# Optimization experiments

Measured on AMD Instinct MI355X. Metric: run time of the kernel, lower is better.

Reference implementation:

```python
import jax, jax.numpy as jnp
import numpy as np

B, LA, LB = 16, 2048, 2048
DA, DB, DH = 768, 512, 512
EPS = 1e-5


def _layer_norm(x, g, b):
    mu = jnp.mean(x, axis=-1, keepdims=True)
    var = jnp.var(x, axis=-1, keepdims=True)
    return (x - mu) * jax.lax.rsqrt(var + EPS) * g + b


def setup_inputs() -> dict:
    key = jax.random.key(0)
    ks = jax.random.split(key, 12)
    s = lambda d: 1.0 / np.sqrt(d)
    return {
        "z_a": jax.random.normal(ks[0], (B, LA, DA), jnp.float32),
        "z_b": jax.random.normal(ks[1], (B, LB, DB), jnp.float32),
        "Wa": jax.random.uniform(ks[2], (DA, DH), jnp.float32, -s(DA), s(DA)),
        "ba": jnp.zeros((DH,), jnp.float32),
        "Wb": jax.random.uniform(ks[3], (DB, DH), jnp.float32, -s(DB), s(DB)),
        "bb": jnp.zeros((DH,), jnp.float32),
        "W_co": jax.random.normal(ks[4], (DH, DH), jnp.float32),
        "Woa": jax.random.uniform(ks[5], (DH, DA), jnp.float32, -s(DH), s(DH)),
        "boa": jnp.zeros((DA,), jnp.float32),
        "Wob": jax.random.uniform(ks[6], (DH, DB), jnp.float32, -s(DH), s(DH)),
        "bob": jnp.zeros((DB,), jnp.float32),
        "ga": jnp.ones((DA,), jnp.float32),
        "beta_a": jnp.zeros((DA,), jnp.float32),
        "gb": jnp.ones((DB,), jnp.float32),
        "beta_b": jnp.zeros((DB,), jnp.float32),
    }


def reference(z_a, z_b, Wa, ba, Wb, bb, W_co, Woa, boa, Wob, bob, ga, beta_a, gb, beta_b):
    # projections to shared hidden space
    h_a = jnp.einsum('bld,dh->blh', z_a, Wa) + ba          # (B, LA, DH)
    h_b = jnp.einsum('bld,dh->blh', z_b, Wb) + bb          # (B, LB, DH)
    # bilinear tanh co-attention scores
    C = jnp.tanh(jnp.einsum('bih,hk,bjk->bij', h_a, W_co, h_b))  # (B, LA, LB)
    attn_a = jax.nn.softmax(C, axis=-1)                    # rows: over LB
    attn_b = jax.nn.softmax(C.transpose(0, 2, 1), axis=-1) # cols: over LA
    h_a_co = jnp.einsum('bij,bjh->bih', attn_a, h_b)       # (B, LA, DH)
    h_b_co = jnp.einsum('bji,bih->bjh', attn_b, h_a)       # (B, LB, DH)
    z_a_co = jnp.einsum('blh,hd->bld', h_a_co, Woa) + boa
    z_b_co = jnp.einsum('blh,hd->bld', h_b_co, Wob) + bob
    z_a_out = _layer_norm(z_a + z_a_co, ga, beta_a)
    z_b_out = _layer_norm(z_b + z_b_co, gb, beta_b)
    return (z_a_out, z_b_out)
```

## Files before the change

### kernel.cpp

```cpp
#include <hip/hip_runtime.h>
#include <stdint.h>

typedef short bf16x8 __attribute__((ext_vector_type(8)));
typedef float f32x16 __attribute__((ext_vector_type(16)));

#define BM 256
#define BN 256
#define BK 64
#define ABUF_U 16384
#define BUF_U  32768

#define AS1 __attribute__((address_space(1)))
#define AS3 __attribute__((address_space(3)))

__device__ __forceinline__ ushort f2bf(float x) {
    uint32_t u = __float_as_uint(x);
    u += 0x7FFFu + ((u >> 16) & 1u);
    return (ushort)(u >> 16);
}

__device__ __forceinline__ void gload16(const void* g, void* l) {
    __builtin_amdgcn_global_load_lds((const AS1 void*)g, (AS3 void*)l, 16, 0, 0);
}

#define ISSUE2(kt, buf, i0)                                                          \
    do {                                                                             \
        gload16(((i0) < 4 ? Ap : Bp) + goff[i0] + (kt), smem + (buf)*BUF_U + loff[i0]); \
        gload16((((i0)+1) < 4 ? Ap : Bp) + goff[(i0)+1] + (kt), smem + (buf)*BUF_U + loff[(i0)+1]); \
    } while (0)

template<int MODE, bool HAS_BIAS, bool WRITE_T>
__global__ __launch_bounds__(512, 2)
void gemm_bt(const ushort* __restrict__ Aptr_, const ushort* __restrict__ Bptr_,
             void* __restrict__ Cptr_, ushort* __restrict__ CTptr_,
             const float* __restrict__ bias, const float* __restrict__ resid_,
             float* __restrict__ rsum_, float* __restrict__ csum_,
             const float* __restrict__ scale_,
             int M, int N, int K, int lda, int ldb, int ldc,
             long sA, long sB, long sC, long sCT, long sSum,
             int ldct, int rbshift)
{
    extern __shared__ ushort smem[];

    const int gx = gridDim.x, gy = gridDim.y;
    const int nwg = gx * gy * (int)gridDim.z;
    int flat = ((int)blockIdx.z * gy + (int)blockIdx.y) * gx + (int)blockIdx.x;
    {
        const int q8 = nwg >> 3, r8 = nwg & 7;
        const int xcd = flat & 7, loc = flat >> 3;
        flat = (xcd < r8 ? xcd * (q8 + 1) : r8 * (q8 + 1) + (xcd - r8) * q8) + loc;
    }
    const int z   = flat / (gx * gy);
    const int rem = flat - z * (gx * gy);
    const int m0  = (rem % gx) * BM;
    const int n0  = (rem / gx) * BN;

    const int tid  = threadIdx.x;
    const int lane = tid & 63;
    const int wave = tid >> 6;
    const int wr   = wave >> 2;
    const int wcn  = wave & 3;
    const int lr   = lane & 31, lh = lane >> 5;

    const ushort* Ap = Aptr_ + z * sA;
    const ushort* Bp = Bptr_ + z * sB;

    long goff[8]; int loff[8];
    #pragma unroll
    for (int u = 0; u < 4; ++u) {
        const int li  = u * 512 + tid;
        const int row = li >> 3;
        const int gck = (li & 7) ^ (row & 7);
        goff[u]     = (long)(m0 + row) * lda + gck * 8;
        loff[u]     = li * 8;
        goff[u + 4] = (long)(n0 + row) * ldb + gck * 8;
        loff[u + 4] = ABUF_U + li * 8;
    }

    f32x16 acc[4][2] = {};

    const int nk = K / BK;
    ISSUE2(0, 0, 0); ISSUE2(0, 0, 2); ISSUE2(0, 0, 4); ISSUE2(0, 0, 6);

    for (int t = 0; t < nk; ++t) {
        const int cur = t & 1, nxt = cur ^ 1;
        const ushort* As = smem + cur * BUF_U;
        const ushort* Bs = As + ABUF_U;
        const bool pf = (t + 1 < nk);
        const int kt1 = (t + 1) * BK;

        if (pf) {
            ISSUE2(kt1, nxt, 0);
            asm volatile("s_waitcnt vmcnt(2)" ::: "memory");
        } else {
            asm volatile("s_waitcnt vmcnt(0)" ::: "memory");
        }
        __builtin_amdgcn_s_barrier();

        #pragma unroll
        for (int kk = 0; kk < 4; ++kk) {
            bf16x8 af[4], bfv[2];
            #pragma unroll
            for (int tm = 0; tm < 4; ++tm) {
                const int row = wr * 128 + tm * 32 + lr;
                const int ck  = (kk * 2 + lh) ^ (row & 7);
                af[tm] = *(const bf16x8*)&As[row * BK + ck * 8];
            }
            #pragma unroll
            for (int tn = 0; tn < 2; ++tn) {
                const int row = wcn * 64 + tn * 32 + lr;
                const int ck  = (kk * 2 + lh) ^ (row & 7);
                bfv[tn] = *(const bf16x8*)&Bs[row * BK + ck * 8];
            }
            if (pf) {
                if (kk == 0)      ISSUE2(kt1, nxt, 2);
                else if (kk == 1) ISSUE2(kt1, nxt, 4);
                else if (kk == 2) ISSUE2(kt1, nxt, 6);
            }
            #pragma unroll
            for (int tm = 0; tm < 4; ++tm)
                #pragma unroll
                for (int tn = 0; tn < 2; ++tn)
                    acc[tm][tn] = __builtin_amdgcn_mfma_f32_32x32x16_bf16(
                        af[tm], bfv[tn], acc[tm][tn], 0, 0, 0);
        }

        asm volatile("s_waitcnt lgkmcnt(0)" ::: "memory");
        __builtin_amdgcn_s_barrier();
    }

    const int colb0 = n0 + wcn * 64 + lr;
    const int rowbw = m0 + wr * 128 + 4 * lh;

    if constexpr (MODE == 3) {
        float* Co = (float*)Cptr_;
        #pragma unroll
        for (int tm = 0; tm < 4; ++tm)
            #pragma unroll
            for (int tn = 0; tn < 2; ++tn) {
                const int col = colb0 + tn * 32;
                const float bv = bias[col];
                #pragma unroll
                for (int q = 0; q < 4; ++q)
                    #pragma unroll
                    for (int s = 0; s < 4; ++s) {
                        const int row = rowbw + tm * 32 + q * 8 + s;
                        const long idx = (long)row * ldc + col;
                        Co[idx] = acc[tm][tn][q * 4 + s] + bv + resid_[idx];
                    }
            }
    } else if constexpr (MODE == 0) {
        ushort* Cp = (ushort*)Cptr_ + z * sC;
        #pragma unroll
        for (int tm = 0; tm < 4; ++tm)
            #pragma unroll
            for (int tn = 0; tn < 2; ++tn) {
                const int col = colb0 + tn * 32;
                const float bv = HAS_BIAS ? bias[col] : 0.f;
                ushort us[16];
                #pragma unroll
                for (int rr = 0; rr < 16; ++rr) us[rr] = f2bf(acc[tm][tn][rr] + bv);
                #pragma unroll
                for (int q = 0; q < 4; ++q)
                    #pragma unroll
                    for (int s = 0; s < 4; ++s)
                        Cp[(long)(rowbw + tm * 32 + q * 8 + s) * ldc + col] = us[q * 4 + s];
                if constexpr (WRITE_T) {
                    #pragma unroll
                    for (int q = 0; q < 4; ++q) {
                        const int gr = rowbw + tm * 32 + q * 8;
                        const int bb = gr >> rbshift;
                        const int ii = gr & ((1 << rbshift) - 1);
                        *(ushort4*)&CTptr_[(long)bb * sCT + (long)col * ldct + ii] =
                            make_ushort4(us[q * 4 + 0], us[q * 4 + 1], us[q * 4 + 2], us[q * 4 + 3]);
                    }
                }
            }
    } else if constexpr (MODE == 1) {
        ushort* Ep  = (ushort*)Cptr_ + z * sC;
        ushort* ETp = CTptr_ + z * sCT;
        float* rs = rsum_ + z * sSum;
        float* cs = csum_ + z * sSum;
        float colp[2] = {0.f, 0.f};
        #pragma unroll
        for (int tm = 0; tm < 4; ++tm) {
            float rowp[16];
            #pragma unroll
            for (int rr = 0; rr < 16; ++rr) rowp[rr] = 0.f;
            #pragma unroll
            for (int tn = 0; tn < 2; ++tn) {
                const int col = colb0 + tn * 32;
                ushort us[16];
                #pragma unroll
                for (int rr = 0; rr < 16; ++rr) {
                    const float x  = acc[tm][tn][rr];
                    const float th = 1.f - 2.f / (__expf(2.f * x) + 1.f);
                    const float e  = __expf(th);
                    rowp[rr] += e;
                    colp[tn] += e;
                    us[rr] = f2bf(e);
                }
                #pragma unroll
                for (int q = 0; q < 4; ++q) {
                    #pragma unroll
                    for (int s = 0; s < 4; ++s)
                        Ep[(long)(rowbw + tm * 32 + q * 8 + s) * ldc + col] = us[q * 4 + s];
                    const int gr = rowbw + tm * 32 + q * 8;
                    *(ushort4*)&ETp[(long)col * ldct + gr] =
                        make_ushort4(us[q * 4 + 0], us[q * 4 + 1], us[q * 4 + 2], us[q * 4 + 3]);
                }
            }
            #pragma unroll
            for (int rr = 0; rr < 16; ++rr) {
                float v = rowp[rr];
                v += __shfl_xor(v, 1);  v += __shfl_xor(v, 2);
                v += __shfl_xor(v, 4);  v += __shfl_xor(v, 8);
                v += __shfl_xor(v, 16);
                if (lr == 0)
                    atomicAdd(&rs[rowbw + tm * 32 + (rr & 3) + 8 * (rr >> 2)], v);
            }
        }
        #pragma unroll
        for (int tn = 0; tn < 2; ++tn) {
            float v = colp[tn];
            v += __shfl_xor(v, 32);
            if (lh == 0) atomicAdd(&cs[colb0 + tn * 32], v);
        }
    } else {
        const float* sc = scale_ + z * sSum;
        ushort* Cp = (ushort*)Cptr_ + z * sC;
        #pragma unroll
        for (int tm = 0; tm < 4; ++tm) {
            float rcp[16];
            #pragma unroll
            for (int rr = 0; rr < 16; ++rr)
                rcp[rr] = 1.f / sc[rowbw + tm * 32 + (rr & 3) + 8 * (rr >> 2)];
            #pragma unroll
            for (int tn = 0; tn < 2; ++tn) {
                const int col = colb0 + tn * 32;
                #pragma unroll
                for (int q = 0; q < 4; ++q)
                    #pragma unroll
                    for (int s = 0; s < 4; ++s)
                        Cp[(long)(rowbw + tm * 32 + q * 8 + s) * ldc + col] =
                            f2bf(acc[tm][tn][q * 4 + s] * rcp[q * 4 + s]);
            }
        }
    }
}

__global__ __launch_bounds__(256)
void cast32to16(const float* __restrict__ in, ushort* __restrict__ out, long n) {
    const long stride = (long)gridDim.x * 256 * 8;
    for (long i = ((long)blockIdx.x * 256 + threadIdx.x) * 8; i < n; i += stride) {
        const float4 f0 = *(const float4*)(in + i);
        const float4 f1 = *(const float4*)(in + i + 4);
        uint4 w;
        w.x = (uint)f2bf(f0.x) | ((uint)f2bf(f0.y) << 16);
        w.y = (uint)f2bf(f0.z) | ((uint)f2bf(f0.w) << 16);
        w.z = (uint)f2bf(f1.x) | ((uint)f2bf(f1.y) << 16);
        w.w = (uint)f2bf(f1.z) | ((uint)f2bf(f1.w) << 16);
        *(uint4*)(out + i) = w;
    }
}

__global__ __launch_bounds__(256)
void tcast(const float* __restrict__ in, ushort* __restrict__ out, int R, int C) {
    __shared__ float t[32][33];
    const int bx = blockIdx.x * 32, by = blockIdx.y * 32;
    const int tx = threadIdx.x, ty = threadIdx.y;
    for (int i = ty; i < 32; i += 8) {
        const int r = by + i, cc = bx + tx;
        if (r < R && cc < C) t[i][tx] = in[(long)r * C + cc];
    }
    __syncthreads();
    for (int i = ty; i < 32; i += 8) {
        const int cc = bx + i, r = by + tx;
        if (cc < C && r < R) out[(long)cc * R + r] = f2bf(t[tx][i]);
    }
}

template<int D>
__global__ __launch_bounds__(256)
void ln_rows(float* __restrict__ y, const float* __restrict__ gam, const float* __restrict__ bet) {
    constexpr int NV = D / 256;
    const long row = blockIdx.x;
    float* p = y + row * D;
    const int tid = threadIdx.x;
    float v[NV];
    float s = 0.f, s2 = 0.f;
    #pragma unroll
    for (int k = 0; k < NV; ++k) {
        v[k] = p[tid + k * 256];
        s += v[k]; s2 += v[k] * v[k];
    }
    #pragma unroll
    for (int off = 1; off < 64; off <<= 1) {
        s  += __shfl_xor(s, off);
        s2 += __shfl_xor(s2, off);
    }
    __shared__ float ws[4], ws2[4];
    const int wave = tid >> 6, lane = tid & 63;
    if (lane == 0) { ws[wave] = s; ws2[wave] = s2; }
    __syncthreads();
    s  = ws[0] + ws[1] + ws[2] + ws[3];
    s2 = ws2[0] + ws2[1] + ws2[2] + ws2[3];
    const float mu  = s / D;
    const float var = s2 / D - mu * mu;
    const float rstd = rsqrtf(var + 1e-5f);
    #pragma unroll
    for (int k = 0; k < NV; ++k) {
        const int i = tid + k * 256;
        p[i] = (v[k] - mu) * rstd * gam[i] + bet[i];
    }
}

extern "C" void kernel_launch(void* const* d_in, const int* in_sizes, int n_in,
                              void* d_out, int out_size, void* d_ws, size_t ws_size,
                              hipStream_t stream)
{
    (void)in_sizes; (void)n_in; (void)out_size; (void)ws_size;
    const float* z_a    = (const float*)d_in[0];
    const float* z_b    = (const float*)d_in[1];
    const float* Wa     = (const float*)d_in[2];
    const float* ba     = (const float*)d_in[3];
    const float* Wb     = (const float*)d_in[4];
    const float* bb     = (const float*)d_in[5];
    const float* Wco    = (const float*)d_in[6];
    const float* Woa    = (const float*)d_in[7];
    const float* boa    = (const float*)d_in[8];
    const float* Wob    = (const float*)d_in[9];
    const float* bob    = (const float*)d_in[10];
    const float* ga     = (const float*)d_in[11];
    const float* beta_a = (const float*)d_in[12];
    const float* gb     = (const float*)d_in[13];
    const float* beta_b = (const float*)d_in[14];

    const int Bn = 16, LA = 2048, LB = 2048, DA = 768, DB = 512, DH = 512;
    const long MA = (long)Bn * LA;
    const long MB = (long)Bn * LB;

    char* w = (char*)d_ws;
    size_t off = 0;
    auto alc = [&](size_t bytes) { void* p = w + off; off += (bytes + 255) & ~(size_t)255; return p; };

    ushort* WaT  = (ushort*)alc((size_t)DH * DA * 2);
    ushort* WbT  = (ushort*)alc((size_t)DH * DB * 2);
    ushort* WcoT = (ushort*)alc((size_t)DH * DH * 2);
    ushort* WoaT = (ushort*)alc((size_t)DA * DH * 2);
    ushort* WobT = (ushort*)alc((size_t)DB * DH * 2);
    ushort* h_a  = (ushort*)alc((size_t)MA * DH * 2);
    ushort* h_b  = (ushort*)alc((size_t)MB * DH * 2);
    ushort* h_aT = (ushort*)alc((size_t)Bn * DH * LA * 2);
    ushort* h_bT = (ushort*)alc((size_t)Bn * DH * LB * 2);
    ushort* Ma   = (ushort*)alc((size_t)MA * DH * 2);
    ushort* E    = (ushort*)alc((size_t)Bn * LA * LB * 2);
    ushort* ET   = (ushort*)alc((size_t)Bn * LB * LA * 2);
    ushort* Pa   = (ushort*)alc((size_t)MA * DH * 2);
    ushort* Pb   = (ushort*)alc((size_t)MB * DH * 2);
    float*  rsum = (float*)alc((size_t)Bn * LA * 4);
    float*  csum = (float*)alc((size_t)Bn * LB * 4);

    ushort* za16 = E;
    ushort* zb16 = E + (size_t)MA * DA;

    dim3 blk(512, 1, 1);
    dim3 blk256(256, 1, 1);
    dim3 tb(32, 8, 1);
    const int SHM = 2 * BUF_U * 2;

    tcast<<<dim3(DH / 32, DA / 32, 1), tb, 0, stream>>>(Wa,  WaT,  DA, DH);
    tcast<<<dim3(DH / 32, DB / 32, 1), tb, 0, stream>>>(Wb,  WbT,  DB, DH);
    tcast<<<dim3(DH / 32, DH / 32, 1), tb, 0, stream>>>(Wco, WcoT, DH, DH);
    tcast<<<dim3(DA / 32, DH / 32, 1), tb, 0, stream>>>(Woa, WoaT, DH, DA);
    tcast<<<dim3(DB / 32, DH / 32, 1), tb, 0, stream>>>(Wob, WobT, DH, DB);

    cast32to16<<<dim3(2048, 1, 1), blk256, 0, stream>>>(z_a, za16, MA * DA);
    cast32to16<<<dim3(2048, 1, 1), blk256, 0, stream>>>(z_b, zb16, MB * DB);

    hipMemsetAsync(rsum, 0, (size_t)Bn * (LA + LB) * sizeof(float), stream);

    gemm_bt<0, true, true><<<dim3(MA / BM, DH / BN, 1), blk, SHM, stream>>>(
        za16, WaT, h_a, h_aT, ba, nullptr, nullptr, nullptr, nullptr,
        (int)MA, DH, DA, DA, DA, DH, 0, 0, 0, (long)DH * LA, 0, LA, 11);

    gemm_bt<0, true, true><<<dim3(MB / BM, DH / BN, 1), blk, SHM, stream>>>(
        zb16, WbT, h_b, h_bT, bb, nullptr, nullptr, nullptr, nullptr,
        (int)MB, DH, DB, DB, DB, DH, 0, 0, 0, (long)DH * LB, 0, LB, 11);

    gemm_bt<0, false, false><<<dim3(MA / BM, DH / BN, 1), blk, SHM, stream>>>(
        h_a, WcoT, Ma, nullptr, nullptr, nullptr, nullptr, nullptr, nullptr,
        (int)MA, DH, DH, DH, DH, DH, 0, 0, 0, 0, 0, 0, 0);

    gemm_bt<1, false, false><<<dim3(LA / BM, LB / BN, Bn), blk, SHM, stream>>>(
        Ma, h_b, E, ET, nullptr, nullptr, rsum, csum, nullptr,
        LA, LB, DH, DH, DH, LB,
        (long)LA * DH, (long)LB * DH, (long)LA * LB, (long)LB * LA, LA, LA, 0);

    gemm_bt<2, false, false><<<dim3(LA / BM, DH / BN, Bn), blk, SHM, stream>>>(
        E, h_bT, Pa, nullptr, nullptr, nullptr, nullptr, nullptr, rsum,
        LA, DH, LB, LB, LB, DH,
        (long)LA * LB, (long)DH * LB, (long)LA * DH, 0, LA, 0, 0);

    gemm_bt<2, false, false><<<dim3(LB / BM, DH / BN, Bn), blk, SHM, stream>>>(
        ET, h_aT, Pb, nullptr, nullptr, nullptr, nullptr, nullptr, csum,
        LB, DH, LA, LA, LA, DH,
        (long)LB * LA, (long)DH * LA, (long)LB * DH, 0, LB, 0, 0);

    float* outA = (float*)d_out;
    float* outB = outA + MA * DA;

    gemm_bt<3, true, false><<<dim3(MA / BM, DA / BN, 1), blk, SHM, stream>>>(
        Pa, WoaT, outA, nullptr, boa, z_a, nullptr, nullptr, nullptr,
        (int)MA, DA, DH, DH, DH, DA, 0, 0, 0, 0, 0, 0, 0);

    gemm_bt<3, true, false><<<dim3(MB / BM, DB / BN, 1), blk, SHM, stream>>>(
        Pb, WobT, outB, nullptr, bob, z_b, nullptr, nullptr, nullptr,
        (int)MB, DB, DH, DH, DH, DB, 0, 0, 0, 0, 0, 0, 0);

    ln_rows<768><<<dim3((unsigned)MA, 1, 1), blk256, 0, stream>>>(outA, ga, beta_a);
    ln_rows<512><<<dim3((unsigned)MB, 1, 1), blk256, 0, stream>>>(outB, gb, beta_b);
}
```

Baseline: 704.6 us.

## Shrink GEMM tiles to 128x128 without prefetch and keep the residual path in bf16

The GEMM kernel drops from 256x256 tiles with 512 threads and a double-buffered async-LDS prefetch pipeline to 128x128 tiles with 256 threads, static single-buffered LDS, and plain syncthreads around each K step. The output projection now writes a bf16 pre-norm sum, using the bf16-cast input as the residual. A new vectorized layernorm kernel reads that bf16 buffer and writes the float result. These changes cut fp32 traffic in the epilogue and layernorm, but they give up load/compute overlap, raise the number of workgroups and redundant operand loads, and lower the accuracy of the residual and the pre-norm sum.

```diff
diff --git a/kernel.cpp b/kernel.cpp
--- a/kernel.cpp
+++ b/kernel.cpp
@@ -4,11 +4,9 @@
 typedef short bf16x8 __attribute__((ext_vector_type(8)));
 typedef float f32x16 __attribute__((ext_vector_type(16)));
 
-#define BM 256
-#define BN 256
+#define BM 128
+#define BN 128
 #define BK 64
-#define ABUF_U 16384
-#define BUF_U  32768
 
 #define AS1 __attribute__((address_space(1)))
 #define AS3 __attribute__((address_space(3)))
@@ -18,29 +16,27 @@
     u += 0x7FFFu + ((u >> 16) & 1u);
     return (ushort)(u >> 16);
 }
+__device__ __forceinline__ float bf2f(ushort u) {
+    return __uint_as_float((uint)u << 16);
+}
 
 __device__ __forceinline__ void gload16(const void* g, void* l) {
     __builtin_amdgcn_global_load_lds((const AS1 void*)g, (AS3 void*)l, 16, 0, 0);
 }
 
-#define ISSUE2(kt, buf, i0)                                                          \
-    do {                                                                             \
-        gload16(((i0) < 4 ? Ap : Bp) + goff[i0] + (kt), smem + (buf)*BUF_U + loff[i0]); \
-        gload16((((i0)+1) < 4 ? Ap : Bp) + goff[(i0)+1] + (kt), smem + (buf)*BUF_U + loff[(i0)+1]); \
-    } while (0)
-
 template<int MODE, bool HAS_BIAS, bool WRITE_T>
-__global__ __launch_bounds__(512, 2)
+__global__ __launch_bounds__(256)
 void gemm_bt(const ushort* __restrict__ Aptr_, const ushort* __restrict__ Bptr_,
              void* __restrict__ Cptr_, ushort* __restrict__ CTptr_,
-             const float* __restrict__ bias, const float* __restrict__ resid_,
+             const float* __restrict__ bias, const ushort* __restrict__ resid_,
              float* __restrict__ rsum_, float* __restrict__ csum_,
              const float* __restrict__ scale_,
              int M, int N, int K, int lda, int ldb, int ldc,
              long sA, long sB, long sC, long sCT, long sSum,
              int ldct, int rbshift)
 {
-    extern __shared__ ushort smem[];
+    __shared__ ushort Alds[BM * BK];
+    __shared__ ushort Blds[BN * BK];
 
     const int gx = gridDim.x, gy = gridDim.y;
     const int nwg = gx * gy * (int)gridDim.z;
@@ -58,84 +54,66 @@
     const int tid  = threadIdx.x;
     const int lane = tid & 63;
     const int wave = tid >> 6;
-    const int wr   = wave >> 2;
-    const int wcn  = wave & 3;
+    const int wr   = wave >> 1;
+    const int wcn  = wave & 1;
     const int lr   = lane & 31, lh = lane >> 5;
 
     const ushort* Ap = Aptr_ + z * sA;
     const ushort* Bp = Bptr_ + z * sB;
 
-    long goff[8]; int loff[8];
+    long aoff[4], boff[4]; int lofs[4];
     #pragma unroll
     for (int u = 0; u < 4; ++u) {
-        const int li  = u * 512 + tid;
+        const int li  = u * 256 + tid;
         const int row = li >> 3;
         const int gck = (li & 7) ^ (row & 7);
-        goff[u]     = (long)(m0 + row) * lda + gck * 8;
-        loff[u]     = li * 8;
-        goff[u + 4] = (long)(n0 + row) * ldb + gck * 8;
-        loff[u + 4] = ABUF_U + li * 8;
-    }
-
-    f32x16 acc[4][2] = {};
-
-    const int nk = K / BK;
-    ISSUE2(0, 0, 0); ISSUE2(0, 0, 2); ISSUE2(0, 0, 4); ISSUE2(0, 0, 6);
-
-    for (int t = 0; t < nk; ++t) {
-        const int cur = t & 1, nxt = cur ^ 1;
-        const ushort* As = smem + cur * BUF_U;
-        const ushort* Bs = As + ABUF_U;
-        const bool pf = (t + 1 < nk);
-        const int kt1 = (t + 1) * BK;
-
-        if (pf) {
-            ISSUE2(kt1, nxt, 0);
-            asm volatile("s_waitcnt vmcnt(2)" ::: "memory");
-        } else {
-            asm volatile("s_waitcnt vmcnt(0)" ::: "memory");
+        aoff[u] = (long)(m0 + row) * lda + gck * 8;
+        boff[u] = (long)(n0 + row) * ldb + gck * 8;
+        lofs[u] = li * 8;
+    }
+
+    f32x16 acc[2][2] = {};
+
+    for (int kt = 0; kt < K; kt += BK) {
+        #pragma unroll
+        for (int u = 0; u < 4; ++u) {
+            gload16(Ap + aoff[u] + kt, &Alds[lofs[u]]);
+            gload16(Bp + boff[u] + kt, &Blds[lofs[u]]);
         }
-        __builtin_amdgcn_s_barrier();
+        __syncthreads();
 
         #pragma unroll
         for (int kk = 0; kk < 4; ++kk) {
-            bf16x8 af[4], bfv[2];
-            #pragma unroll
-            for (int tm = 0; tm < 4; ++tm) {
-                const int row = wr * 128 + tm * 32 + lr;
+            bf16x8 af[2], bfv[2];
+            #pragma unroll
+            for (int tm = 0; tm < 2; ++tm) {
+                const int row = wr * 64 + tm * 32 + lr;
                 const int ck  = (kk * 2 + lh) ^ (row & 7);
-                af[tm] = *(const bf16x8*)&As[row * BK + ck * 8];
+                af[tm] = *(const bf16x8*)&Alds[row * BK + ck * 8];
             }
             #pragma unroll
             for (int tn = 0; tn < 2; ++tn) {
                 const int row = wcn * 64 + tn * 32 + lr;
                 const int ck  = (kk * 2 + lh) ^ (row & 7);
-                bfv[tn] = *(const bf16x8*)&Bs[row * BK + ck * 8];
-            }
-            if (pf) {
-                if (kk == 0)      ISSUE2(kt1, nxt, 2);
-                else if (kk == 1) ISSUE2(kt1, nxt, 4);
-                else if (kk == 2) ISSUE2(kt1, nxt, 6);
-            }
-            #pragma unroll
-            for (int tm = 0; tm < 4; ++tm)
+                bfv[tn] = *(const bf16x8*)&Blds[row * BK + ck * 8];
+            }
+            #pragma unroll
+            for (int tm = 0; tm < 2; ++tm)
                 #pragma unroll
                 for (int tn = 0; tn < 2; ++tn)
                     acc[tm][tn] = __builtin_amdgcn_mfma_f32_32x32x16_bf16(
                         af[tm], bfv[tn], acc[tm][tn], 0, 0, 0);
         }
-
-        asm volatile("s_waitcnt lgkmcnt(0)" ::: "memory");
-        __builtin_amdgcn_s_barrier();
+        __syncthreads();
     }
 
     const int colb0 = n0 + wcn * 64 + lr;
-    const int rowbw = m0 + wr * 128 + 4 * lh;
+    const int rowbw = m0 + wr * 64 + 4 * lh;
 
     if constexpr (MODE == 3) {
-        float* Co = (float*)Cptr_;
-        #pragma unroll
-        for (int tm = 0; tm < 4; ++tm)
+        ushort* Cp = (ushort*)Cptr_;
+        #pragma unroll
+        for (int tm = 0; tm < 2; ++tm)
             #pragma unroll
             for (int tn = 0; tn < 2; ++tn) {
                 const int col = colb0 + tn * 32;
@@ -146,13 +124,13 @@
                     for (int s = 0; s < 4; ++s) {
                         const int row = rowbw + tm * 32 + q * 8 + s;
                         const long idx = (long)row * ldc + col;
-                        Co[idx] = acc[tm][tn][q * 4 + s] + bv + resid_[idx];
+                        Cp[idx] = f2bf(acc[tm][tn][q * 4 + s] + bv + bf2f(resid_[idx]));
                     }
             }
     } else if constexpr (MODE == 0) {
         ushort* Cp = (ushort*)Cptr_ + z * sC;
         #pragma unroll
-        for (int tm = 0; tm < 4; ++tm)
+        for (int tm = 0; tm < 2; ++tm)
             #pragma unroll
             for (int tn = 0; tn < 2; ++tn) {
                 const int col = colb0 + tn * 32;
@@ -183,7 +161,7 @@
         float* cs = csum_ + z * sSum;
         float colp[2] = {0.f, 0.f};
         #pragma unroll
-        for (int tm = 0; tm < 4; ++tm) {
+        for (int tm = 0; tm < 2; ++tm) {
             float rowp[16];
             #pragma unroll
             for (int rr = 0; rr < 16; ++rr) rowp[rr] = 0.f;
@@ -230,7 +208,7 @@
         const float* sc = scale_ + z * sSum;
         ushort* Cp = (ushort*)Cptr_ + z * sC;
         #pragma unroll
-        for (int tm = 0; tm < 4; ++tm) {
+        for (int tm = 0; tm < 2; ++tm) {
             float rcp[16];
             #pragma unroll
             for (int rr = 0; rr < 16; ++rr)
@@ -281,19 +259,16 @@
 }
 
 template<int D>
-__global__ __launch_bounds__(256)
-void ln_rows(float* __restrict__ y, const float* __restrict__ gam, const float* __restrict__ bet) {
-    constexpr int NV = D / 256;
+__global__ __launch_bounds__(D / 4)
+void ln_bf(const ushort* __restrict__ y, float* __restrict__ out,
+           const float* __restrict__ gam, const float* __restrict__ bet) {
+    constexpr int NW = D / 256;
     const long row = blockIdx.x;
-    float* p = y + row * D;
     const int tid = threadIdx.x;
-    float v[NV];
-    float s = 0.f, s2 = 0.f;
-    #pragma unroll
-    for (int k = 0; k < NV; ++k) {
-        v[k] = p[tid + k * 256];
-        s += v[k]; s2 += v[k] * v[k];
-    }
+    const ushort4 v4 = *(const ushort4*)&y[row * D + tid * 4];
+    float v[4] = {bf2f(v4.x), bf2f(v4.y), bf2f(v4.z), bf2f(v4.w)};
+    float s = v[0] + v[1] + v[2] + v[3];
+    float s2 = v[0]*v[0] + v[1]*v[1] + v[2]*v[2] + v[3]*v[3];
     #pragma unroll
     for (int off = 1; off < 64; off <<= 1) {
         s  += __shfl_xor(s, off);
@@ -303,16 +278,20 @@
     const int wave = tid >> 6, lane = tid & 63;
     if (lane == 0) { ws[wave] = s; ws2[wave] = s2; }
     __syncthreads();
-    s  = ws[0] + ws[1] + ws[2] + ws[3];
-    s2 = ws2[0] + ws2[1] + ws2[2] + ws2[3];
-    const float mu  = s / D;
-    const float var = s2 / D - mu * mu;
+    s = 0.f; s2 = 0.f;
+    #pragma unroll
+    for (int w2 = 0; w2 < NW; ++w2) { s += ws[w2]; s2 += ws2[w2]; }
+    const float mu   = s / D;
+    const float var  = s2 / D - mu * mu;
     const float rstd = rsqrtf(var + 1e-5f);
-    #pragma unroll
-    for (int k = 0; k < NV; ++k) {
-        const int i = tid + k * 256;
-        p[i] = (v[k] - mu) * rstd * gam[i] + bet[i];
-    }
+    const float4 gv = *(const float4*)&gam[tid * 4];
+    const float4 bv = *(const float4*)&bet[tid * 4];
+    float4 o;
+    o.x = (v[0] - mu) * rstd * gv.x + bv.x;
+    o.y = (v[1] - mu) * rstd * gv.y + bv.y;
+    o.z = (v[2] - mu) * rstd * gv.z + bv.z;
+    o.w = (v[3] - mu) * rstd * gv.w + bv.w;
+    *(float4*)&out[row * D + tid * 4] = o;
 }
 
 extern "C" void kernel_launch(void* const* d_in, const int* in_sizes, int n_in,
@@ -361,13 +340,13 @@
     float*  rsum = (float*)alc((size_t)Bn * LA * 4);
     float*  csum = (float*)alc((size_t)Bn * LB * 4);
 
-    ushort* za16 = E;
-    ushort* zb16 = E + (size_t)MA * DA;
-
-    dim3 blk(512, 1, 1);
-    dim3 blk256(256, 1, 1);
+    ushort* za16 = (ushort*)d_out;
+    ushort* zb16 = za16 + (size_t)MA * DA;
+    ushort* yA = E;
+    ushort* yB = E + (size_t)MA * DA;
+
+    dim3 blk(256, 1, 1);
     dim3 tb(32, 8, 1);
-    const int SHM = 2 * BUF_U * 2;
 
     tcast<<<dim3(DH / 32, DA / 32, 1), tb, 0, stream>>>(Wa,  WaT,  DA, DH);
     tcast<<<dim3(DH / 32, DB / 32, 1), tb, 0, stream>>>(Wb,  WbT,  DB, DH);
@@ -375,49 +354,48 @@
     tcast<<<dim3(DA / 32, DH / 32, 1), tb, 0, stream>>>(Woa, WoaT, DH, DA);
     tcast<<<dim3(DB / 32, DH / 32, 1), tb, 0, stream>>>(Wob, WobT, DH, DB);
 
-    cast32to16<<<dim3(2048, 1, 1), blk256, 0, stream>>>(z_a, za16, MA * DA);
-    cast32to16<<<dim3(2048, 1, 1), blk256, 0, stream>>>(z_b, zb16, MB * DB);
+    cast32to16<<<dim3(2048, 1, 1), blk, 0, stream>>>(z_a, za16, MA * DA);
+    cast32to16<<<dim3(2048, 1, 1), blk, 0, stream>>>(z_b, zb16, MB * DB);
 
     hipMemsetAsync(rsum, 0, (size_t)Bn * (LA + LB) * sizeof(float), stream);
 
-    gemm_bt<0, true, true><<<dim3(MA / BM, DH / BN, 1), blk, SHM, stream>>>(
+    gemm_bt<0, true, true><<<dim3(MA / BM, DH / BN, 1), blk, 0, stream>>>(
         za16, WaT, h_a, h_aT, ba, nullptr, nullptr, nullptr, nullptr,
         (int)MA, DH, DA, DA, DA, DH, 0, 0, 0, (long)DH * LA, 0, LA, 11);
 
-    gemm_bt<0, true, true><<<dim3(MB / BM, DH / BN, 1), blk, SHM, stream>>>(
+    gemm_bt<0, true, true><<<dim3(MB / BM, DH / BN, 1), blk, 0, stream>>>(
         zb16, WbT, h_b, h_bT, bb, nullptr, nullptr, nullptr, nullptr,
         (int)MB, DH, DB, DB, DB, DH, 0, 0, 0, (long)DH * LB, 0, LB, 11);
 
-    gemm_bt<0, false, false><<<dim3(MA / BM, DH / BN, 1), blk, SHM, stream>>>(
+    gemm_bt<0, false, false><<<dim3(MA / BM, DH / BN, 1), blk, 0, stream>>>(
         h_a, WcoT, Ma, nullptr, nullptr, nullptr, nullptr, nullptr, nullptr,
         (int)MA, DH, DH, DH, DH, DH, 0, 0, 0, 0, 0, 0, 0);
 
-    gemm_bt<1, false, false><<<dim3(LA / BM, LB / BN, Bn), blk, SHM, stream>>>(
+    gemm_bt<1, false, false><<<dim3(LA / BM, LB / BN, Bn), blk, 0, stream>>>(
         Ma, h_b, E, ET, nullptr, nullptr, rsum, csum, nullptr,
         LA, LB, DH, DH, DH, LB,
         (long)LA * DH, (long)LB * DH, (long)LA * LB, (long)LB * LA, LA, LA, 0);
 
-    gemm_bt<2, false, false><<<dim3(LA / BM, DH / BN, Bn), blk, SHM, stream>>>(
+    gemm_bt<2, false, false><<<dim3(LA / BM, DH / BN, Bn), blk, 0, stream>>>(
         E, h_bT, Pa, nullptr, nullptr, nullptr, nullptr, nullptr, rsum,
         LA, DH, LB, LB, LB, DH,
         (long)LA * LB, (long)DH * LB, (long)LA * DH, 0, LA, 0, 0);
 
-    gemm_bt<2, false, false><<<dim3(LB / BM, DH / BN, Bn), blk, SHM, stream>>>(
+    gemm_bt<2, false, false><<<dim3(LB / BM, DH / BN, Bn), blk, 0, stream>>>(
         ET, h_aT, Pb, nullptr, nullptr, nullptr, nullptr, nullptr, csum,
         LB, DH, LA, LA, LA, DH,
         (long)LB * LA, (long)DH * LA, (long)LB * DH, 0, LB, 0, 0);
 
+    gemm_bt<3, true, false><<<dim3(MA / BM, DA / BN, 1), blk, 0, stream>>>(
+        Pa, WoaT, yA, nullptr, boa, za16, nullptr, nullptr, nullptr,
+        (int)MA, DA, DH, DH, DH, DA, 0, 0, 0, 0, 0, 0, 0);
+
+    gemm_bt<3, true, false><<<dim3(MB / BM, DB / BN, 1), blk, 0, stream>>>(
+        Pb, WobT, yB, nullptr, bob, zb16, nullptr, nullptr, nullptr,
+        (int)MB, DB, DH, DH, DH, DB, 0, 0, 0, 0, 0, 0, 0);
+
     float* outA = (float*)d_out;
     float* outB = outA + MA * DA;
-
-    gemm_bt<3, true, false><<<dim3(MA / BM, DA / BN, 1), blk, SHM, stream>>>(
-        Pa, WoaT, outA, nullptr, boa, z_a, nullptr, nullptr, nullptr,
-        (int)MA, DA, DH, DH, DH, DA, 0, 0, 0, 0, 0, 0, 0);
-
-    gemm_bt<3, true, false><<<dim3(MB / BM, DB / BN, 1), blk, SHM, stream>>>(
-        Pb, WobT, outB, nullptr, bob, z_b, nullptr, nullptr, nullptr,
-        (int)MB, DB, DH, DH, DH, DB, 0, 0, 0, 0, 0, 0, 0);
-
-    ln_rows<768><<<dim3((unsigned)MA, 1, 1), blk256, 0, stream>>>(outA, ga, beta_a);
-    ln_rows<512><<<dim3((unsigned)MB, 1, 1), blk256, 0, stream>>>(outB, gb, beta_b);
-}
+    ln_bf<768><<<dim3((unsigned)MA, 1, 1), dim3(192, 1, 1), 0, stream>>>(yA, outA, ga, beta_a);
+    ln_bf<512><<<dim3((unsigned)MB, 1, 1), dim3(128, 1, 1), 0, stream>>>(yB, outB, gb, beta_b);
+}
```

Measured after the change: 810.0 us. 15.0% more time.
